# Kernel tuning notes

Hardware: AMD Instinct MI355X
Metric: run time of the kernel (lower is better)

## Reference

```python
import jax, jax.numpy as jnp
import numpy as np

H = 64  # hidden_size


def _lstm_layer(x, Wih, Whh, bih, bhh):
    """One LSTM layer, batch_first. x: [B,T,I] -> h_seq: [B,T,H].
    PyTorch gate order: i, f, g, o."""
    B = x.shape[0]
    # Precompute input contribution for all timesteps: [B,T,4H]
    xg = jnp.einsum('bti,gi->btg', x, Wih) + bih + bhh
    xg = jnp.swapaxes(xg, 0, 1)  # [T,B,4H] for scan

    def step(carry, xg_t):
        h, c = carry
        gates = xg_t + h @ Whh.T  # [B,4H]
        i, f, g, o = jnp.split(gates, 4, axis=-1)
        i = jax.nn.sigmoid(i)
        f = jax.nn.sigmoid(f)
        g = jnp.tanh(g)
        o = jax.nn.sigmoid(o)
        c = f * c + i * g
        h = o * jnp.tanh(c)
        return (h, c), h

    h0 = jnp.zeros((B, H), dtype=x.dtype)
    c0 = jnp.zeros((B, H), dtype=x.dtype)
    (_, _), h_seq = jax.lax.scan(step, (h0, c0), xg)
    return jnp.swapaxes(h_seq, 0, 1)  # [B,T,H]


def setup_inputs() -> dict:
    key = jax.random.key(0)
    ks = jax.random.split(key, 11)
    B, T, I, O = 2048, 512, 6, 6
    s = 1.0 / np.sqrt(H)
    u = lambda k, shape: jax.random.uniform(k, shape, jnp.float32, -s, s)
    return {
        'x': jax.random.normal(ks[0], (B, T, I), jnp.float32),
        'Wih0': u(ks[1], (4 * H, I)),
        'Whh0': u(ks[2], (4 * H, H)),
        'bih0': u(ks[3], (4 * H,)),
        'bhh0': u(ks[4], (4 * H,)),
        'Wih1': u(ks[5], (4 * H, H)),
        'Whh1': u(ks[6], (4 * H, H)),
        'bih1': u(ks[7], (4 * H,)),
        'bhh1': u(ks[8], (4 * H,)),
        'Wlin': u(ks[9], (O, H)),
        'blin': u(ks[10], (O,)),
    }


def reference(x, Wih0, Whh0, bih0, bhh0, Wih1, Whh1, bih1, bhh1, Wlin, blin):
    h1 = _lstm_layer(x, Wih0, Whh0, bih0, bhh0)   # [B,T,H]
    h2 = _lstm_layer(h1, Wih1, Whh1, bih1, bhh1)  # [B,T,H]
    return h2[:, -1, :] @ Wlin.T + blin           # [B,O]
```

## Files before the change

### kernel.cpp

```cpp
#include <hip/hip_runtime.h>

typedef _Float16 f16;
typedef _Float16 f16x2 __attribute__((ext_vector_type(2)));
typedef _Float16 f16x4 __attribute__((ext_vector_type(4)));
typedef _Float16 f16x8 __attribute__((ext_vector_type(8)));
typedef float f32x4 __attribute__((ext_vector_type(4)));

#define LOG2E 1.4426950408889634f
#define C2LE  2.8853900817779268f

__device__ __forceinline__ float fastrcp(float x) { return __builtin_amdgcn_rcpf(x); }
__device__ __forceinline__ float fexp2(float x) { return __builtin_amdgcn_exp2f(x); }

#define TT 512
#define NB 8
#define XBS 3080
#define XS_ELE (NB * XBS)
#define AUGS 184
#define A0OFF XS_ELE
#define A1OFF (A0OFF + NB * AUGS)
#define LDS_F16 (A1OFF + NB * AUGS)
#define LDS_BYTES (LDS_F16 * 2)

__device__ __forceinline__ f16x8 cvt8s(const float* p, float s) {
  f32x4 a = *(const f32x4*)p;
  f32x4 b = *(const f32x4*)(p + 4);
  f16x8 r;
  #pragma unroll
  for (int i = 0; i < 4; ++i) { r[i] = (f16)(a[i] * s); r[4 + i] = (f16)(b[i] * s); }
  return r;
}

__global__ __launch_bounds__(512, 2)
void lstm2_kernel(const float* __restrict__ x,
                  const float* __restrict__ Wih0, const float* __restrict__ Whh0,
                  const float* __restrict__ bih0, const float* __restrict__ bhh0,
                  const float* __restrict__ Wih1, const float* __restrict__ Whh1,
                  const float* __restrict__ bih1, const float* __restrict__ bhh1,
                  const float* __restrict__ Wlin, const float* __restrict__ blin,
                  float* __restrict__ out)
{
  extern __shared__ f16 lds[];
  f16* xstage = lds;
  f16* aug0 = lds + A0OFF;
  f16* aug1 = lds + A1OFF;
  const unsigned int* xw = (const unsigned int*)xstage;

  const int tid = threadIdx.x;
  const int wv = tid >> 6;
  const int team = wv >> 2;
  const int uw = wv & 3;
  const int lane = tid & 63;
  const int m = lane & 15;
  const int q = lane >> 4;
  const bool lohalf = (m < 8);
  const int bcol = m & 7;

  f16x8 af[4][4];
  f32x4 bv[4];
  #pragma unroll
  for (int g = 0; g < 4; ++g) {
    const float sg = (g == 2) ? C2LE : LOG2E;
    const int R = g * 64 + 16 * uw + m;
    if (team == 1) {
      af[g][0] = cvt8s(&Whh1[R * 64 + 8 * q], sg);
      af[g][1] = cvt8s(&Whh1[R * 64 + 32 + 8 * q], sg);
      af[g][2] = cvt8s(&Wih1[R * 64 + 8 * q], sg);
      af[g][3] = cvt8s(&Wih1[R * 64 + 32 + 8 * q], sg);
    } else {
      af[g][0] = cvt8s(&Whh0[R * 64 + 8 * q], sg);
      af[g][1] = cvt8s(&Whh0[R * 64 + 32 + 8 * q], sg);
      f16x8 t;
      #pragma unroll
      for (int i = 0; i < 8; ++i) t[i] = (f16)0.0f;
      if (q == 0) {
        #pragma unroll
        for (int i = 0; i < 6; ++i) t[i] = (f16)(Wih0[R * 6 + i] * sg);
      }
      af[g][2] = t;
      af[g][3] = t;
    }
    const float* bi = (team == 1) ? bih1 : bih0;
    const float* bh = (team == 1) ? bhh1 : bhh0;
    const int U = g * 64 + 16 * uw + 4 * q;
    #pragma unroll
    for (int r = 0; r < 4; ++r) bv[g][r] = (bi[U + r] + bh[U + r]) * sg;
  }

  {
    const float* xblk = x + (size_t)blockIdx.x * (NB * TT * 6);
    #pragma unroll 1
    for (int n = 0; n < NB; ++n) {
      const float* src = xblk + n * (TT * 6);
      f16* dst = xstage + n * XBS;
      for (int idx = tid; idx < TT * 6 / 4; idx += 512) {
        f32x4 v = *(const f32x4*)&src[idx * 4];
        f16x4 h;
        #pragma unroll
        for (int i = 0; i < 4; ++i) h[i] = (f16)v[i];
        *(f16x4*)&dst[idx * 4] = h;
      }
    }
  }
  for (int idx = tid; idx < NB * AUGS; idx += 512) aug0[idx] = (f16)0.0f;
  __syncthreads();

  float cs0 = 0.0f, cs1 = 0.0f;

  const int colb = bcol * AUGS;
  const int xdw = bcol * (XBS / 2);
  const int rowofs = 16 * uw + 4 * q + (lohalf ? 0 : 2);

  auto finish1 = [&](float ai, float afv, float ag, float ao, float& cs) -> f16 {
    float A = 1.0f + fexp2(-ai);
    float B = 1.0f + fexp2(-afv);
    float G = 1.0f + fexp2(-ag);
    float O = 1.0f + fexp2(-ao);
    float d1 = fastrcp(A * B);
    float d2 = fastrcp(G * O);
    float si = d1 * B;
    float sf = d1 * A;
    float tg = 2.0f * (d2 * O) - 1.0f;
    float so = d2 * G;
    float cn = __builtin_fmaf(sf, cs, si * tg);
    cs = cn;
    float T = 1.0f + fexp2(cn * -C2LE);
    float th = 2.0f * fastrcp(T) - 1.0f;
    return (f16)(so * th);
  };

  auto compact_finish = [&](const f32x4* acc) -> f16x2 {
    float u0[4], u1[4];
    #pragma unroll
    for (int g = 0; g < 4; ++g) {
      u0[g] = lohalf ? acc[g][0] : acc[g][2];
      u1[g] = lohalf ? acc[g][1] : acc[g][3];
    }
    f16x2 ho;
    ho[0] = finish1(u0[0], u0[1], u0[2], u0[3], cs0);
    ho[1] = finish1(u1[0], u1[1], u1[2], u1[3], cs1);
    return ho;
  };

  if (team == 0) {
    union { unsigned int u[4]; f16x8 h; } bx;
    bx.u[0] = xw[xdw + 0]; bx.u[1] = xw[xdw + 1]; bx.u[2] = xw[xdw + 2]; bx.u[3] = 0u;
    f32x4 acc[4];
    #pragma unroll
    for (int g = 0; g < 4; ++g)
      acc[g] = __builtin_amdgcn_mfma_f32_16x16x32_f16(af[g][2], bx.h, bv[g], 0, 0, 0);
    f16x2 h1o = compact_finish(acc);
    *(f16x2*)&aug0[colb + 64 + rowofs] = h1o;
  }
  __syncthreads();

  f16* cur = aug0;
  f16* nxt = aug1;
  #pragma unroll 1
  for (int t = 0; t < TT - 1; ++t) {
    f16x8 Bh1a = *(const f16x8*)&cur[colb + 64 + 8 * q];
    f16x8 Bh1b = *(const f16x8*)&cur[colb + 96 + 8 * q];
    if (team == 1) {
      f16x8 Bh2a = *(const f16x8*)&cur[colb + 0 + 8 * q];
      f16x8 Bh2b = *(const f16x8*)&cur[colb + 32 + 8 * q];
      f32x4 acc[4];
      __builtin_amdgcn_s_setprio(1);
      #pragma unroll
      for (int g = 0; g < 4; ++g) {
        f32x4 p = __builtin_amdgcn_mfma_f32_16x16x32_f16(af[g][0], Bh2a, bv[g], 0, 0, 0);
        p = __builtin_amdgcn_mfma_f32_16x16x32_f16(af[g][1], Bh2b, p, 0, 0, 0);
        p = __builtin_amdgcn_mfma_f32_16x16x32_f16(af[g][2], Bh1a, p, 0, 0, 0);
        acc[g] = __builtin_amdgcn_mfma_f32_16x16x32_f16(af[g][3], Bh1b, p, 0, 0, 0);
      }
      __builtin_amdgcn_s_setprio(0);
      f16x2 h2o = compact_finish(acc);
      *(f16x2*)&nxt[colb + rowofs] = h2o;
    } else {
      union { unsigned int u[4]; f16x8 h; } bx;
      const int xo = xdw + 3 * (t + 1);
      bx.u[0] = xw[xo]; bx.u[1] = xw[xo + 1]; bx.u[2] = xw[xo + 2]; bx.u[3] = 0u;
      f32x4 acc[4];
      __builtin_amdgcn_s_setprio(1);
      #pragma unroll
      for (int g = 0; g < 4; ++g) {
        f32x4 p = __builtin_amdgcn_mfma_f32_16x16x32_f16(af[g][0], Bh1a, bv[g], 0, 0, 0);
        p = __builtin_amdgcn_mfma_f32_16x16x32_f16(af[g][1], Bh1b, p, 0, 0, 0);
        acc[g] = __builtin_amdgcn_mfma_f32_16x16x32_f16(af[g][2], bx.h, p, 0, 0, 0);
      }
      __builtin_amdgcn_s_setprio(0);
      f16x2 h1o = compact_finish(acc);
      *(f16x2*)&nxt[colb + 64 + rowofs] = h1o;
    }
    __syncthreads();
    f16* tmp = cur; cur = nxt; nxt = tmp;
  }

  if (team == 1) {
    f16x8 Bh2a = *(const f16x8*)&cur[colb + 0 + 8 * q];
    f16x8 Bh2b = *(const f16x8*)&cur[colb + 32 + 8 * q];
    f16x8 Bh1a = *(const f16x8*)&cur[colb + 64 + 8 * q];
    f16x8 Bh1b = *(const f16x8*)&cur[colb + 96 + 8 * q];
    f32x4 acc[4];
    #pragma unroll
    for (int g = 0; g < 4; ++g) {
      f32x4 p = __builtin_amdgcn_mfma_f32_16x16x32_f16(af[g][0], Bh2a, bv[g], 0, 0, 0);
      p = __builtin_amdgcn_mfma_f32_16x16x32_f16(af[g][1], Bh2b, p, 0, 0, 0);
      p = __builtin_amdgcn_mfma_f32_16x16x32_f16(af[g][2], Bh1a, p, 0, 0, 0);
      acc[g] = __builtin_amdgcn_mfma_f32_16x16x32_f16(af[g][3], Bh1b, p, 0, 0, 0);
    }
    f16x2 h2o = compact_finish(acc);
    *(f16x2*)&nxt[colb + rowofs] = h2o;
  }
  __syncthreads();

  if (tid < 48) {
    const int bl = tid / 6, o = tid - bl * 6;
    float s = blin[o];
    const float* wl = &Wlin[o * 64];
    #pragma unroll 8
    for (int u = 0; u < 64; ++u) s += wl[u] * (float)nxt[bl * AUGS + u];
    out[(blockIdx.x * NB + bl) * 6 + o] = s;
  }
}

extern "C" void kernel_launch(void* const* d_in, const int* in_sizes, int n_in,
                              void* d_out, int out_size, void* d_ws, size_t ws_size,
                              hipStream_t stream) {
  const float* xp    = (const float*)d_in[0];
  const float* Wih0  = (const float*)d_in[1];
  const float* Whh0  = (const float*)d_in[2];
  const float* bih0  = (const float*)d_in[3];
  const float* bhh0  = (const float*)d_in[4];
  const float* Wih1  = (const float*)d_in[5];
  const float* Whh1  = (const float*)d_in[6];
  const float* bih1  = (const float*)d_in[7];
  const float* bhh1  = (const float*)d_in[8];
  const float* Wlin  = (const float*)d_in[9];
  const float* blin  = (const float*)d_in[10];
  float* outp = (float*)d_out;

  hipFuncSetAttribute(reinterpret_cast<const void*>(lstm2_kernel),
                      hipFuncAttributeMaxDynamicSharedMemorySize, LDS_BYTES);
  lstm2_kernel<<<256, 512, LDS_BYTES, stream>>>(xp, Wih0, Whh0, bih0, bhh0,
                                                Wih1, Whh1, bih1, bhh1,
                                                Wlin, blin, outp);
}
```

Before: 293.9 us.

## Halve batch per block and remap lanes to one hidden unit each

Reduces the batch columns per block from 8 to 4 and doubles the grid so two blocks can share each CU. Lanes that held duplicate MFMA columns now each take a distinct row of the 4-row output slice, so every lane evaluates one LSTM cell instead of two. The aim is to shorten the per-timestep activation tail on the serial critical path and improve CU occupancy. In exchange, the MFMA work per block is unchanged while the useful columns are halved, and two blocks compete for each CU.

```diff
diff --git a/kernel.cpp b/kernel.cpp
--- a/kernel.cpp
+++ b/kernel.cpp
@@ -13,7 +13,7 @@
 __device__ __forceinline__ float fexp2(float x) { return __builtin_amdgcn_exp2f(x); }
 
 #define TT 512
-#define NB 8
+#define NB 4
 #define XBS 3080
 #define XS_ELE (NB * XBS)
 #define AUGS 184
@@ -53,8 +53,10 @@
   const int lane = tid & 63;
   const int m = lane & 15;
   const int q = lane >> 4;
-  const bool lohalf = (m < 8);
-  const int bcol = m & 7;
+  const int bcol = m & 3;
+  const int s0 = (m >> 2) & 1;
+  const int s1 = (m >> 3) & 1;
+  const int sub = m >> 2;
 
   f16x8 af[4][4];
   f32x4 bv[4];
@@ -105,13 +107,13 @@
   for (int idx = tid; idx < NB * AUGS; idx += 512) aug0[idx] = (f16)0.0f;
   __syncthreads();
 
-  float cs0 = 0.0f, cs1 = 0.0f;
+  float cs = 0.0f;
 
   const int colb = bcol * AUGS;
   const int xdw = bcol * (XBS / 2);
-  const int rowofs = 16 * uw + 4 * q + (lohalf ? 0 : 2);
-
-  auto finish1 = [&](float ai, float afv, float ag, float ao, float& cs) -> f16 {
+  const int rowofs = 16 * uw + 4 * q + sub;
+
+  auto finish1 = [&](float ai, float afv, float ag, float ao) -> f16 {
     float A = 1.0f + fexp2(-ai);
     float B = 1.0f + fexp2(-afv);
     float G = 1.0f + fexp2(-ag);
@@ -129,28 +131,25 @@
     return (f16)(so * th);
   };
 
-  auto compact_finish = [&](const f32x4* acc) -> f16x2 {
-    float u0[4], u1[4];
+  auto compact_finish = [&](const f32x4* acc) -> f16 {
+    float u[4];
     #pragma unroll
     for (int g = 0; g < 4; ++g) {
-      u0[g] = lohalf ? acc[g][0] : acc[g][2];
-      u1[g] = lohalf ? acc[g][1] : acc[g][3];
-    }
-    f16x2 ho;
-    ho[0] = finish1(u0[0], u0[1], u0[2], u0[3], cs0);
-    ho[1] = finish1(u1[0], u1[1], u1[2], u1[3], cs1);
-    return ho;
+      float lo = s0 ? acc[g][1] : acc[g][0];
+      float hi = s0 ? acc[g][3] : acc[g][2];
+      u[g] = s1 ? hi : lo;
+    }
+    return finish1(u[0], u[1], u[2], u[3]);
   };
 
   if (team == 0) {
-    union { unsigned int u[4]; f16x8 h; } bx;
-    bx.u[0] = xw[xdw + 0]; bx.u[1] = xw[xdw + 1]; bx.u[2] = xw[xdw + 2]; bx.u[3] = 0u;
+    union { unsigned int un[4]; f16x8 h; } bx;
+    bx.un[0] = xw[xdw + 0]; bx.un[1] = xw[xdw + 1]; bx.un[2] = xw[xdw + 2]; bx.un[3] = 0u;
     f32x4 acc[4];
     #pragma unroll
     for (int g = 0; g < 4; ++g)
       acc[g] = __builtin_amdgcn_mfma_f32_16x16x32_f16(af[g][2], bx.h, bv[g], 0, 0, 0);
-    f16x2 h1o = compact_finish(acc);
-    *(f16x2*)&aug0[colb + 64 + rowofs] = h1o;
+    aug0[colb + 64 + rowofs] = compact_finish(acc);
   }
   __syncthreads();
 
@@ -173,12 +172,11 @@
         acc[g] = __builtin_amdgcn_mfma_f32_16x16x32_f16(af[g][3], Bh1b, p, 0, 0, 0);
       }
       __builtin_amdgcn_s_setprio(0);
-      f16x2 h2o = compact_finish(acc);
-      *(f16x2*)&nxt[colb + rowofs] = h2o;
+      nxt[colb + rowofs] = compact_finish(acc);
     } else {
-      union { unsigned int u[4]; f16x8 h; } bx;
+      union { unsigned int un[4]; f16x8 h; } bx;
       const int xo = xdw + 3 * (t + 1);
-      bx.u[0] = xw[xo]; bx.u[1] = xw[xo + 1]; bx.u[2] = xw[xo + 2]; bx.u[3] = 0u;
+      bx.un[0] = xw[xo]; bx.un[1] = xw[xo + 1]; bx.un[2] = xw[xo + 2]; bx.un[3] = 0u;
       f32x4 acc[4];
       __builtin_amdgcn_s_setprio(1);
       #pragma unroll
@@ -188,8 +186,7 @@
         acc[g] = __builtin_amdgcn_mfma_f32_16x16x32_f16(af[g][2], bx.h, p, 0, 0, 0);
       }
       __builtin_amdgcn_s_setprio(0);
-      f16x2 h1o = compact_finish(acc);
-      *(f16x2*)&nxt[colb + 64 + rowofs] = h1o;
+      nxt[colb + 64 + rowofs] = compact_finish(acc);
     }
     __syncthreads();
     f16* tmp = cur; cur = nxt; nxt = tmp;
@@ -208,12 +205,11 @@
       p = __builtin_amdgcn_mfma_f32_16x16x32_f16(af[g][2], Bh1a, p, 0, 0, 0);
       acc[g] = __builtin_amdgcn_mfma_f32_16x16x32_f16(af[g][3], Bh1b, p, 0, 0, 0);
     }
-    f16x2 h2o = compact_finish(acc);
-    *(f16x2*)&nxt[colb + rowofs] = h2o;
+    nxt[colb + rowofs] = compact_finish(acc);
   }
   __syncthreads();
 
-  if (tid < 48) {
+  if (tid < 24) {
     const int bl = tid / 6, o = tid - bl * 6;
     float s = blin[o];
     const float* wl = &Wlin[o * 64];
@@ -241,7 +237,7 @@
 
   hipFuncSetAttribute(reinterpret_cast<const void*>(lstm2_kernel),
                       hipFuncAttributeMaxDynamicSharedMemorySize, LDS_BYTES);
-  lstm2_kernel<<<256, 512, LDS_BYTES, stream>>>(xp, Wih0, Whh0, bih0, bhh0,
+  lstm2_kernel<<<512, 512, LDS_BYTES, stream>>>(xp, Wih0, Whh0, bih0, bhh0,
                                                 Wih1, Whh1, bih1, bhh1,
                                                 Wlin, blin, outp);
 }
```

Measured after the change: 433.6 us. 1.48x slower.
